# Kernel optimization log

Hardware: AMD Instinct MI355X
Metric: run time of the kernel (lower is better)

## Reference

```python
import jax, jax.numpy as jnp
import numpy as np

N, E = 50000, 800000
F_IN, EDGE_DIM, H, C = 128, 64, 8, 32
NEG_SLOPE = 0.2


def setup_inputs() -> dict:
    key = jax.random.key(0)
    ks = jax.random.split(key, 9)
    return {
        "x": jax.random.normal(ks[0], (N, F_IN), dtype=jnp.float32),
        "edge_index": jax.random.randint(ks[1], (2, E), 0, N, dtype=jnp.int32),
        "edge_attr": jax.random.normal(ks[2], (E, EDGE_DIM), dtype=jnp.float32),
        "W": jax.random.normal(ks[3], (F_IN, H * C), dtype=jnp.float32) * 0.05,
        "att_src": jax.random.normal(ks[4], (H, C), dtype=jnp.float32) * 0.05,
        "att_dst": jax.random.normal(ks[5], (H, C), dtype=jnp.float32) * 0.05,
        "W_edge": jax.random.normal(ks[6], (EDGE_DIM, H * C), dtype=jnp.float32) * 0.05,
        "att_edge": jax.random.normal(ks[7], (H, C), dtype=jnp.float32) * 0.05,
        "bias": jax.random.normal(ks[8], (H * C,), dtype=jnp.float32) * 0.05,
    }


def reference(x, edge_index, edge_attr, W, att_src, att_dst, W_edge, att_edge, bias):
    src, dst = edge_index[0], edge_index[1]  # messages flow src -> dst
    # Pre-activation ReLU from Graph_intra.forward
    xr = jax.nn.relu(x)
    # Linear projection, per-head view: [N, H, C]
    xs = (xr @ W).reshape(N, H, C)
    # Per-node attention logits: [N, H]
    a_src = jnp.einsum("nhc,hc->nh", xs, att_src)
    a_dst = jnp.einsum("nhc,hc->nh", xs, att_dst)
    # Edge-feature attention contribution: [E, H]
    e_proj = (edge_attr @ W_edge).reshape(E, H, C)
    a_edge = jnp.einsum("ehc,hc->eh", e_proj, att_edge)
    # Per-edge logits + LeakyReLU
    alpha = jax.nn.leaky_relu(a_src[src] + a_dst[dst] + a_edge, NEG_SLOPE)  # [E, H]
    # Segment softmax over destination neighborhoods
    seg_max = jax.ops.segment_max(alpha, dst, num_segments=N)
    seg_max = jnp.where(jnp.isfinite(seg_max), seg_max, 0.0)
    alpha = jnp.exp(alpha - seg_max[dst])
    seg_sum = jax.ops.segment_sum(alpha, dst, num_segments=N)
    alpha = alpha / (seg_sum[dst] + 1e-16)
    # Weighted message aggregation: scatter-add alpha_e * x_src[e]
    msgs = alpha[:, :, None] * xs[src]  # [E, H, C]
    out = jax.ops.segment_sum(msgs, dst, num_segments=N)  # [N, H, C]
    return out.reshape(N, H * C) + bias
```

## Files before the change

### kernel.cpp

```cpp
#include <hip/hip_runtime.h>

#define N_NODES 50000
#define E_EDGES 800000
#define F_IN    128
#define EDGE_DIM 64
#define HC      256
#define NEG_SLOPE 0.2f

typedef __attribute__((ext_vector_type(8))) short short8;
typedef __attribute__((ext_vector_type(4))) float f32x4;

__device__ __forceinline__ unsigned short f2bf(float f) {
    unsigned u = __builtin_bit_cast(unsigned, f);
    u += 0x7fffu + ((u >> 16) & 1u);
    return (unsigned short)(u >> 16);
}
__device__ __forceinline__ float bf2f(unsigned short b) {
    return __builtin_bit_cast(float, (unsigned)b << 16);
}

__global__ __launch_bounds__(256) void k_pre(const float* __restrict__ W,
        const float* __restrict__ att_src, const float* __restrict__ att_dst,
        const float* __restrict__ W_edge, const float* __restrict__ att_edge,
        unsigned short* __restrict__ W_T, unsigned short* __restrict__ WaT,
        float* __restrict__ We_fold, int* __restrict__ counts, int* __restrict__ gcur) {
    int idx = blockIdx.x * 256 + threadIdx.x;
    if (idx < N_NODES) counts[idx] = 0;
    if (idx == 0) *gcur = 0;
    if (idx < 32768) {
        int n = idx >> 7, k = idx & 127;
        W_T[n * 128 + k] = f2bf(W[k * 256 + n]);
    }
    if (idx < 2048) {
        int col = idx & 15, k = idx >> 4;
        const float* att = (col < 8) ? att_src : att_dst;
        int h = col & 7;
        float s = 0.f;
        #pragma unroll
        for (int c = 0; c < 32; ++c)
            s = fmaf(W[k * 256 + h * 32 + c], att[h * 32 + c], s);
        WaT[col * 128 + k] = f2bf(s);
    }
    if (idx < 512) {
        int d = idx >> 3, h = idx & 7;
        float s = 0.f;
        #pragma unroll
        for (int c = 0; c < 32; ++c)
            s = fmaf(W_edge[d * 256 + h * 32 + c], att_edge[h * 32 + c], s);
        We_fold[d * 8 + h] = s;
    }
}

#define NT_TILES 782
#define K1_GRID 512
#define HIST_BLOCKS 782
__global__ __launch_bounds__(256, 2) void k1h(const float* __restrict__ x,
        const unsigned short* __restrict__ W_T, const unsigned short* __restrict__ WaT,
        const int4* __restrict__ dst4, int* __restrict__ counts, int4* __restrict__ slot4,
        unsigned short* __restrict__ xs, float* __restrict__ a_src, float* __restrict__ a_dst) {
    __shared__ unsigned short sB[256 * 128];
    __shared__ unsigned short sA[64 * 128];
    int t = threadIdx.x;

    if (blockIdx.x < HIST_BLOCKS) {
        int i = blockIdx.x * 256 + t;
        if (i < E_EDGES / 4) {
            int4 d = dst4[i];
            int4 sl;
            sl.x = atomicAdd(&counts[d.x], 1);
            sl.y = atomicAdd(&counts[d.y], 1);
            sl.z = atomicAdd(&counts[d.z], 1);
            sl.w = atomicAdd(&counts[d.w], 1);
            slot4[i] = sl;
        }
        return;
    }
    int bid = blockIdx.x - HIST_BLOCKS;

    for (int G = t; G < 4096; G += 256) {
        int n = G >> 4, gi = G & 15;
        *(int4*)&sB[(n * 16 + (gi ^ (n & 7))) * 8] = *(const int4*)&W_T[n * 128 + gi * 8];
    }
    int lane = t & 63, w = t >> 6, mr = lane & 15, g = lane >> 4;
    short8 wa[4];
    #pragma unroll
    for (int ks = 0; ks < 4; ++ks)
        wa[ks] = *(const short8*)&WaT[mr * 128 + ks * 32 + g * 8];

    bool first = true;
    for (int rt = bid; rt < NT_TILES; rt += K1_GRID) {
        if (!first) __syncthreads();
        first = false;
        for (int G = t; G < 1024; G += 256) {
            int r = G >> 4, gi = G & 15;
            int node = rt * 64 + r;
            unsigned short pk[8];
            if (node < N_NODES) {
                const float* xp = &x[(long)node * 128 + gi * 8];
                #pragma unroll
                for (int jj = 0; jj < 8; ++jj) pk[jj] = f2bf(fmaxf(xp[jj], 0.f));
            } else {
                #pragma unroll
                for (int jj = 0; jj < 8; ++jj) pk[jj] = 0;
            }
            *(int4*)&sA[(r * 16 + (gi ^ (r & 7))) * 8] = *(int4*)pk;
        }
        __syncthreads();

        f32x4 acc[17];
        #pragma unroll
        for (int i = 0; i < 17; ++i) acc[i] = (f32x4){0.f, 0.f, 0.f, 0.f};

        int r16 = w * 16 + mr;
        #pragma unroll
        for (int ks = 0; ks < 4; ++ks) {
            int pos = (ks * 4 + g) ^ (mr & 7);
            short8 a = *(const short8*)&sA[(r16 * 16 + pos) * 8];
            #pragma unroll
            for (int nt = 0; nt < 16; ++nt) {
                short8 b = *(const short8*)&sB[((nt * 16 + mr) * 16 + pos) * 8];
                acc[nt] = __builtin_amdgcn_mfma_f32_16x16x32_bf16(a, b, acc[nt], 0, 0, 0);
            }
            acc[16] = __builtin_amdgcn_mfma_f32_16x16x32_bf16(a, wa[ks], acc[16], 0, 0, 0);
        }

        #pragma unroll
        for (int r = 0; r < 4; ++r) {
            int node = rt * 64 + w * 16 + g * 4 + r;
            if (node < N_NODES) {
                #pragma unroll
                for (int nt = 0; nt < 16; ++nt)
                    xs[(long)node * 256 + nt * 16 + mr] = f2bf(acc[nt][r]);
                if (mr < 8) a_src[node * 8 + mr]       = acc[16][r];
                else        a_dst[node * 8 + (mr - 8)] = acc[16][r];
            }
        }
    }
}

__global__ __launch_bounds__(256) void k4_alloc(const int* __restrict__ counts,
                                                int* __restrict__ starts,
                                                int* __restrict__ gcur) {
    int n = blockIdx.x * 256 + threadIdx.x;
    int c = (n < N_NODES) ? counts[n] : 0;
    int incl = c;
    #pragma unroll
    for (int off = 1; off < 64; off <<= 1) {
        int u = __shfl_up(incl, off);
        if ((threadIdx.x & 63) >= off) incl += u;
    }
    int total = __shfl(incl, 63);
    int wavebase = 0;
    if ((threadIdx.x & 63) == 63) wavebase = atomicAdd(gcur, total);
    wavebase = __shfl(wavebase, 63);
    if (n < N_NODES) starts[n] = wavebase + incl - c;
}

__global__ __launch_bounds__(256) void k25_fused(const float4* __restrict__ edge_attr4,
        const float* __restrict__ We_fold,
        const int* __restrict__ src, const int* __restrict__ dst,
        const int* __restrict__ slot, const int* __restrict__ starts,
        const float* __restrict__ a_src, const float* __restrict__ a_dst,
        _Float16* __restrict__ w_perm, int* __restrict__ src_perm) {
    __shared__ __align__(16) float se[32 * 68];
    __shared__ __align__(16) float sfT[8 * 68];
    __shared__ int s_src[32], s_dstn[32], s_pos[32];
    int t = threadIdx.x;
    long ebase = (long)blockIdx.x * 32;
    for (int i = t; i < 512; i += 256)
        sfT[(i & 7) * 68 + (i >> 3)] = We_fold[i];
    for (int i = t; i < 512; i += 256) {
        float4 v = edge_attr4[ebase * 16 + i];
        *(float4*)&se[(i >> 4) * 68 + (i & 15) * 4] = v;
    }
    if (t < 32) {
        int ee = ebase + t;
        int dn = dst[ee];
        s_dstn[t] = dn;
        s_src[t] = src[ee];
        s_pos[t] = starts[dn] + slot[ee];
    }
    __syncthreads();
    int e = t >> 3, h = t & 7;
    const float4* sa = (const float4*)&se[e * 68];
    const float4* sb = (const float4*)&sfT[h * 68];
    float s = 0.f;
    #pragma unroll
    for (int i = 0; i < 16; ++i) {
        float4 a = sa[i], b = sb[i];
        s = fmaf(a.x, b.x, s);
        s = fmaf(a.y, b.y, s);
        s = fmaf(a.z, b.z, s);
        s = fmaf(a.w, b.w, s);
    }
    int sn = s_src[e], dn = s_dstn[e];
    float v = s + a_src[sn * 8 + h] + a_dst[dn * 8 + h];
    v = (v > 0.f) ? v : NEG_SLOPE * v;
    float w = __expf(v);
    int pos = s_pos[e];
    w_perm[(size_t)pos * 8 + h] = (_Float16)w;
    if (h == 0) src_perm[pos] = sn;
}

__global__ __launch_bounds__(256) void k6_wave(
    const int* __restrict__ starts, const int* __restrict__ counts,
    const _Float16* __restrict__ w_perm, const int* __restrict__ src_perm,
    const unsigned short* __restrict__ xs, const float* __restrict__ bias,
    float* __restrict__ out) {
    int lane = threadIdx.x & 63;
    int n = blockIdx.x * 4 + (threadIdx.x >> 6);
    if (n >= N_NODES) return;
    int start = starts[n], cnt = counts[n];
    int j = lane >> 3;
    int hq = lane >> 3;

    float acc0 = 0.f, acc1 = 0.f, acc2 = 0.f, acc3 = 0.f;
    float psum = 0.f;
    for (int base = 0; base < cnt; base += 8) {
        int nk = cnt - base; if (nk > 8) nk = 8;
        float wv = (float)w_perm[(size_t)(start + base) * 8 + lane];
        if (j >= nk) wv = 0.f;
        psum += wv;
        int sv = src_perm[start + base + (lane & 7)];
        #pragma unroll
        for (int jj = 0; jj < 8; ++jj) {
            int s = __shfl(sv, jj);
            s = (jj < nk) ? s : 0;
            float w = __shfl(wv, jj * 8 + hq);
            ushort4 xv = *(const ushort4*)&xs[(size_t)s * 256 + lane * 4];
            acc0 = fmaf(w, bf2f(xv.x), acc0);
            acc1 = fmaf(w, bf2f(xv.y), acc1);
            acc2 = fmaf(w, bf2f(xv.z), acc2);
            acc3 = fmaf(w, bf2f(xv.w), acc3);
        }
    }
    psum += __shfl_xor(psum, 8);
    psum += __shfl_xor(psum, 16);
    psum += __shfl_xor(psum, 32);
    float denom = __shfl(psum, hq);
    float rinv = 1.0f / (denom + 1e-16f);
    float4 bv = *(const float4*)&bias[lane * 4];
    f32x4 o;
    o[0] = acc0 * rinv + bv.x;
    o[1] = acc1 * rinv + bv.y;
    o[2] = acc2 * rinv + bv.z;
    o[3] = acc3 * rinv + bv.w;
    __builtin_nontemporal_store(o, (f32x4*)&out[(size_t)n * 256 + lane * 4]);
}

extern "C" void kernel_launch(void* const* d_in, const int* in_sizes, int n_in,
                              void* d_out, int out_size, void* d_ws, size_t ws_size,
                              hipStream_t stream) {
    const float* x         = (const float*)d_in[0];
    const int*   ei        = (const int*)d_in[1];
    const float* edge_attr = (const float*)d_in[2];
    const float* W         = (const float*)d_in[3];
    const float* att_src   = (const float*)d_in[4];
    const float* att_dst   = (const float*)d_in[5];
    const float* W_edge    = (const float*)d_in[6];
    const float* att_edge  = (const float*)d_in[7];
    const float* bias      = (const float*)d_in[8];
    float* out = (float*)d_out;

    const int* e_src = ei;
    const int* e_dst = ei + E_EDGES;

    char* p = (char*)d_ws;
    unsigned short* xs = (unsigned short*)p; p += (size_t)N_NODES * HC * 2;
    float* a_src   = (float*)p; p += (size_t)N_NODES * 8 * 4;
    float* a_dst   = (float*)p; p += (size_t)N_NODES * 8 * 4;
    _Float16* w_perm = (_Float16*)p; p += (size_t)E_EDGES * 8 * 2 + 256;
    int* src_perm  = (int*)p;   p += (size_t)E_EDGES * 4 + 256;
    int* slot      = (int*)p;   p += (size_t)E_EDGES * 4 + 256;
    unsigned short* W_T  = (unsigned short*)p; p += 32768 * 2;
    unsigned short* WaT  = (unsigned short*)p; p += 2048 * 2;
    float* We_fold = (float*)p; p += 512 * 4;
    int* counts    = (int*)p;   p += 200192;
    int* starts    = (int*)p;   p += 200192;
    int* gcur      = (int*)p;   p += 256;

    hipLaunchKernelGGL(k_pre, dim3(196), dim3(256), 0, stream,
                       W, att_src, att_dst, W_edge, att_edge, W_T, WaT, We_fold, counts, gcur);
    hipLaunchKernelGGL(k1h, dim3(HIST_BLOCKS + K1_GRID), dim3(256), 0, stream,
                       x, W_T, WaT, (const int4*)e_dst, counts, (int4*)slot, xs, a_src, a_dst);
    hipLaunchKernelGGL(k4_alloc, dim3(196), dim3(256), 0, stream,
                       counts, starts, gcur);
    hipLaunchKernelGGL(k25_fused, dim3(E_EDGES / 32), dim3(256), 0, stream,
                       (const float4*)edge_attr, We_fold, e_src, e_dst, slot, starts,
                       a_src, a_dst, w_perm, src_perm);
    hipLaunchKernelGGL(k6_wave, dim3(N_NODES / 4), dim3(256), 0, stream,
                       starts, counts, w_perm, src_perm, xs, bias, out);
}
```

Before: 208.5 us.

## Compute edge attention logits with bf16 MFMA instead of scalar FMA

The edge-logit kernel now converts edge_attr rows to bf16 in registers and multiplies them against a folded, zero-padded 16x64 bf16 edge-attention matrix using 16x16x32 MFMA, instead of staging fp32 rows in shared memory and doing scalar dot products. Each block now handles 256 edges rather than 32, with one edge per thread for index and permutation lookups. The edge_attr read (about 200MB) dominates, so the compute change matters less than the access pattern. Each lane reads 8 contiguous floats per row, which may coalesce worse than the old float4 staging. The bf16 rounding of the attributes and weights also lowers the precision of the logits.

```diff
diff --git a/kernel.cpp b/kernel.cpp
--- a/kernel.cpp
+++ b/kernel.cpp
@@ -23,7 +23,7 @@
         const float* __restrict__ att_src, const float* __restrict__ att_dst,
         const float* __restrict__ W_edge, const float* __restrict__ att_edge,
         unsigned short* __restrict__ W_T, unsigned short* __restrict__ WaT,
-        float* __restrict__ We_fold, int* __restrict__ counts, int* __restrict__ gcur) {
+        unsigned short* __restrict__ WaE, int* __restrict__ counts, int* __restrict__ gcur) {
     int idx = blockIdx.x * 256 + threadIdx.x;
     if (idx < N_NODES) counts[idx] = 0;
     if (idx == 0) *gcur = 0;
@@ -41,13 +41,15 @@
             s = fmaf(W[k * 256 + h * 32 + c], att[h * 32 + c], s);
         WaT[col * 128 + k] = f2bf(s);
     }
-    if (idx < 512) {
-        int d = idx >> 3, h = idx & 7;
+    if (idx < 1024) {
+        int c = idx >> 6, k = idx & 63;
         float s = 0.f;
-        #pragma unroll
-        for (int c = 0; c < 32; ++c)
-            s = fmaf(W_edge[d * 256 + h * 32 + c], att_edge[h * 32 + c], s);
-        We_fold[d * 8 + h] = s;
+        if (c < 8) {
+            #pragma unroll
+            for (int cc = 0; cc < 32; ++cc)
+                s = fmaf(W_edge[k * 256 + c * 32 + cc], att_edge[c * 32 + cc], s);
+        }
+        WaE[c * 64 + k] = (c < 8) ? f2bf(s) : (unsigned short)0;
     }
 }
 
@@ -156,50 +158,52 @@
     if (n < N_NODES) starts[n] = wavebase + incl - c;
 }
 
-__global__ __launch_bounds__(256) void k25_fused(const float4* __restrict__ edge_attr4,
-        const float* __restrict__ We_fold,
+__global__ __launch_bounds__(256) void k25_mfma(const float* __restrict__ ea,
+        const unsigned short* __restrict__ WaE,
         const int* __restrict__ src, const int* __restrict__ dst,
         const int* __restrict__ slot, const int* __restrict__ starts,
         const float* __restrict__ a_src, const float* __restrict__ a_dst,
         _Float16* __restrict__ w_perm, int* __restrict__ src_perm) {
-    __shared__ __align__(16) float se[32 * 68];
-    __shared__ __align__(16) float sfT[8 * 68];
-    __shared__ int s_src[32], s_dstn[32], s_pos[32];
+    __shared__ int s_sn[256], s_dn[256], s_pos[256];
     int t = threadIdx.x;
-    long ebase = (long)blockIdx.x * 32;
-    for (int i = t; i < 512; i += 256)
-        sfT[(i & 7) * 68 + (i >> 3)] = We_fold[i];
-    for (int i = t; i < 512; i += 256) {
-        float4 v = edge_attr4[ebase * 16 + i];
-        *(float4*)&se[(i >> 4) * 68 + (i & 15) * 4] = v;
-    }
-    if (t < 32) {
-        int ee = ebase + t;
-        int dn = dst[ee];
-        s_dstn[t] = dn;
-        s_src[t] = src[ee];
-        s_pos[t] = starts[dn] + slot[ee];
+    int blockbase = blockIdx.x * 256;
+    {
+        int e = blockbase + t;
+        int dn = dst[e], sn = src[e];
+        int pos = starts[dn] + slot[e];
+        s_sn[t] = sn; s_dn[t] = dn; s_pos[t] = pos;
+        src_perm[pos] = sn;
     }
     __syncthreads();
-    int e = t >> 3, h = t & 7;
-    const float4* sa = (const float4*)&se[e * 68];
-    const float4* sb = (const float4*)&sfT[h * 68];
-    float s = 0.f;
+    int lane = t & 63, w = t >> 6;
+    int mr = lane & 15, g = lane >> 4;
+    short8 b0 = *(const short8*)&WaE[mr * 64 + g * 8];
+    short8 b1 = *(const short8*)&WaE[mr * 64 + 32 + g * 8];
+
     #pragma unroll
-    for (int i = 0; i < 16; ++i) {
-        float4 a = sa[i], b = sb[i];
-        s = fmaf(a.x, b.x, s);
-        s = fmaf(a.y, b.y, s);
-        s = fmaf(a.z, b.z, s);
-        s = fmaf(a.w, b.w, s);
-    }
-    int sn = s_src[e], dn = s_dstn[e];
-    float v = s + a_src[sn * 8 + h] + a_dst[dn * 8 + h];
-    v = (v > 0.f) ? v : NEG_SLOPE * v;
-    float w = __expf(v);
-    int pos = s_pos[e];
-    w_perm[(size_t)pos * 8 + h] = (_Float16)w;
-    if (h == 0) src_perm[pos] = sn;
+    for (int ti = 0; ti < 4; ++ti) {
+        int lb = w * 64 + ti * 16;
+        int er = blockbase + lb + mr;
+        const float* ap = &ea[(size_t)er * 64 + g * 8];
+        short8 a0, a1;
+        #pragma unroll
+        for (int j = 0; j < 8; ++j) a0[j] = (short)f2bf(ap[j]);
+        #pragma unroll
+        for (int j = 0; j < 8; ++j) a1[j] = (short)f2bf(ap[32 + j]);
+        f32x4 acc = (f32x4){0.f, 0.f, 0.f, 0.f};
+        acc = __builtin_amdgcn_mfma_f32_16x16x32_bf16(a0, b0, acc, 0, 0, 0);
+        acc = __builtin_amdgcn_mfma_f32_16x16x32_bf16(a1, b1, acc, 0, 0, 0);
+        if (mr < 8) {
+            #pragma unroll
+            for (int r = 0; r < 4; ++r) {
+                int le = lb + g * 4 + r;
+                int sn = s_sn[le], dn = s_dn[le];
+                float v = acc[r] + a_src[sn * 8 + mr] + a_dst[dn * 8 + mr];
+                v = (v > 0.f) ? v : NEG_SLOPE * v;
+                w_perm[(size_t)s_pos[le] * 8 + mr] = (_Float16)__expf(v);
+            }
+        }
+    }
 }
 
 __global__ __launch_bounds__(256) void k6_wave(
@@ -274,19 +278,19 @@
     int* slot      = (int*)p;   p += (size_t)E_EDGES * 4 + 256;
     unsigned short* W_T  = (unsigned short*)p; p += 32768 * 2;
     unsigned short* WaT  = (unsigned short*)p; p += 2048 * 2;
-    float* We_fold = (float*)p; p += 512 * 4;
+    unsigned short* WaE  = (unsigned short*)p; p += 1024 * 2;
     int* counts    = (int*)p;   p += 200192;
     int* starts    = (int*)p;   p += 200192;
     int* gcur      = (int*)p;   p += 256;
 
     hipLaunchKernelGGL(k_pre, dim3(196), dim3(256), 0, stream,
-                       W, att_src, att_dst, W_edge, att_edge, W_T, WaT, We_fold, counts, gcur);
+                       W, att_src, att_dst, W_edge, att_edge, W_T, WaT, WaE, counts, gcur);
     hipLaunchKernelGGL(k1h, dim3(HIST_BLOCKS + K1_GRID), dim3(256), 0, stream,
                        x, W_T, WaT, (const int4*)e_dst, counts, (int4*)slot, xs, a_src, a_dst);
     hipLaunchKernelGGL(k4_alloc, dim3(196), dim3(256), 0, stream,
                        counts, starts, gcur);
-    hipLaunchKernelGGL(k25_fused, dim3(E_EDGES / 32), dim3(256), 0, stream,
-                       (const float4*)edge_attr, We_fold, e_src, e_dst, slot, starts,
+    hipLaunchKernelGGL(k25_mfma, dim3(E_EDGES / 256), dim3(256), 0, stream,
+                       edge_attr, WaE, e_src, e_dst, slot, starts,
                        a_src, a_dst, w_perm, src_perm);
     hipLaunchKernelGGL(k6_wave, dim3(N_NODES / 4), dim3(256), 0, stream,
                        starts, counts, w_perm, src_perm, xs, bias, out);
```

New measurement: 209.3 us (median of 2 runs). Within noise of the previous version (+0.4%).
